# Kernel tuning notes

Measured on AMD Instinct MI355X. Metric: run time of the kernel, lower is better.

Reference implementation:

```python
import jax, jax.numpy as jnp
import numpy as np
import math

EMBED = 1024
HEADS = 16
HEAD_DIM = EMBED // HEADS
B, Hh, Ww = 256, 10, 10
MAX_POS = 100


def setup_inputs() -> dict:
    key = jax.random.key(0)
    ks = jax.random.split(key, 10)
    s = 1.0 / math.sqrt(EMBED)
    return {
        "x": jax.random.normal(ks[0], (B, EMBED, Hh, Ww), dtype=jnp.float32),
        "Wq": jax.random.uniform(ks[1], (EMBED, EMBED), jnp.float32, -s, s),
        "bq": jax.random.uniform(ks[2], (EMBED,), jnp.float32, -s, s),
        "Wk": jax.random.uniform(ks[3], (EMBED, EMBED), jnp.float32, -s, s),
        "bk": jax.random.uniform(ks[4], (EMBED,), jnp.float32, -s, s),
        "Wv": jax.random.uniform(ks[5], (EMBED, EMBED), jnp.float32, -s, s),
        "bv": jax.random.uniform(ks[6], (EMBED,), jnp.float32, -s, s),
        "Wo": jax.random.uniform(ks[7], (EMBED, EMBED), jnp.float32, -s, s),
        "bo": jax.random.uniform(ks[8], (EMBED,), jnp.float32, -s, s),
        "pos_encoding": jax.random.normal(ks[9], (MAX_POS, EMBED), dtype=jnp.float32),
    }


def reference(x, Wq, bq, Wk, bk, Wv, bv, Wo, bo, pos_encoding):
    # x: [B, E, H, W]
    b, e, h, w = x.shape
    s = h * w  # seq_len
    scale = math.sqrt(HEAD_DIM)
    x_flat = x.reshape(b, e, s).transpose(0, 2, 1)  # [B, S, E]
    x_flat = x_flat + pos_encoding[:s][None]  # broadcast over batch
    q = x_flat @ Wq + bq
    k = x_flat @ Wk + bk
    v = x_flat @ Wv + bv
    # [B, H, S, D]
    q = q.reshape(b, s, HEADS, HEAD_DIM).transpose(0, 2, 1, 3)
    k = k.reshape(b, s, HEADS, HEAD_DIM).transpose(0, 2, 1, 3)
    v = v.reshape(b, s, HEADS, HEAD_DIM).transpose(0, 2, 1, 3)
    scores = jnp.einsum('bhqd,bhkd->bhqk', q, k) / scale
    attn = jax.nn.softmax(scores, axis=-1)  # dropout = identity (eval)
    attended = jnp.einsum('bhqk,bhkd->bhqd', attn, v)
    attended = attended.transpose(0, 2, 1, 3).reshape(b, s, e)
    out = attended @ Wo + bo
    out = out.transpose(0, 2, 1).reshape(b, e, h, w)
    return out, attn
```

## Files before the change

### kernel.cpp

```cpp
#include <hip/hip_runtime.h>

typedef unsigned short u16;
typedef __attribute__((ext_vector_type(8))) short short8;
typedef __attribute__((ext_vector_type(4))) float f32x4;

#define BATCH 256
#define S_LEN 100
#define EMB   1024
#define NHEAD 16
#define HDIM  64

__device__ __forceinline__ float b2f(u16 h) {
  union { unsigned u; float f; } v; v.u = ((unsigned)h) << 16; return v.f;
}
__device__ __forceinline__ u16 f2bf(float f) {
  union { float f; unsigned u; } v; v.f = f;
  unsigned r = v.u + 0x7fffu + ((v.u >> 16) & 1u);
  return (u16)(r >> 16);
}

__device__ __forceinline__ void gld_lds16(const u16* g, u16* l) {
  __builtin_amdgcn_global_load_lds((const __attribute__((address_space(1))) void*)g,
                                   (__attribute__((address_space(3))) void*)l,
                                   16, 0, 0);
}

#define MFMA16(a, b, c) __builtin_amdgcn_mfma_f32_16x16x32_bf16(a, b, c, 0, 0, 0)

__global__ __launch_bounds__(256) void w_xpose(
    const float* __restrict__ Wq, const float* __restrict__ Wk,
    const float* __restrict__ Wv, const float* __restrict__ Wo,
    u16* __restrict__ WtQ, u16* __restrict__ WtK,
    u16* __restrict__ WtV, u16* __restrict__ WtO)
{
  __shared__ u16 tile[64 * 73];
  int z = blockIdx.z;
  const float* W = (z == 0) ? Wq : (z == 1) ? Wk : (z == 2) ? Wv : Wo;
  u16* Wt        = (z == 0) ? WtQ : (z == 1) ? WtK : (z == 2) ? WtV : WtO;
  int k0 = blockIdx.x * 64, n0 = blockIdx.y * 64;
  for (int idx = threadIdx.x; idx < 4096; idx += 256) {
    int r = idx >> 6, c = idx & 63;
    tile[r * 73 + c] = f2bf(W[(size_t)(k0 + r) * EMB + n0 + c]);
  }
  __syncthreads();
  for (int idx = threadIdx.x; idx < 4096; idx += 256) {
    int c = idx >> 6, r = idx & 63;
    Wt[(size_t)(n0 + c) * EMB + k0 + r] = tile[r * 73 + c];
  }
}

__global__ __launch_bounds__(256) void xpose_pos(
    const float* __restrict__ x, const float* __restrict__ pos, u16* __restrict__ xT)
{
  __shared__ float tile[64 * 105];
  int e0 = blockIdx.x * 64;
  int b  = blockIdx.y;
  const float* xb = x + (size_t)b * EMB * S_LEN;
  for (int idx = threadIdx.x; idx < 6400; idx += 256) {
    int i = idx / 100, s = idx - i * 100;
    tile[i * 105 + s] = xb[(size_t)(e0 + i) * S_LEN + s];
  }
  __syncthreads();
  for (int idx = threadIdx.x; idx < 6400; idx += 256) {
    int s = idx >> 6, i = idx & 63;
    float v = tile[i * 105 + s] + pos[(size_t)s * EMB + e0 + i];
    xT[(size_t)b * (S_LEN * EMB) + (size_t)s * EMB + e0 + i] = f2bf(v);
  }
}

__global__ __launch_bounds__(256) void out_xpose(
    const u16* __restrict__ tmp, float* __restrict__ out)
{
  __shared__ u16 tile[100 * 73];
  int e0 = blockIdx.x * 64;
  int b  = blockIdx.y;
  for (int idx = threadIdx.x; idx < 6400; idx += 256) {
    int s = idx >> 6, i = idx & 63;
    tile[s * 73 + i] = tmp[(size_t)b * (S_LEN * EMB) + (size_t)s * EMB + e0 + i];
  }
  __syncthreads();
  for (int idx = threadIdx.x; idx < 6400; idx += 256) {
    int i = idx / 100, s = idx - i * 100;
    out[((size_t)b * EMB + e0 + i) * S_LEN + s] = b2f(tile[s * 73 + i]);
  }
}

__global__ __launch_bounds__(512) void gemm256(
    const u16* __restrict__ A,
    const u16* __restrict__ Bt0, const u16* __restrict__ Bt1, const u16* __restrict__ Bt2,
    const float* __restrict__ bias0, const float* __restrict__ bias1, const float* __restrict__ bias2,
    u16* __restrict__ C0, u16* __restrict__ C1, u16* __restrict__ C2)
{
  __shared__ u16 lds[5 * 16384];

  const int z = blockIdx.z;
  const u16* Bt     = (z == 0) ? Bt0 : (z == 1) ? Bt1 : Bt2;
  const float* bias = (z == 0) ? bias0 : (z == 1) ? bias1 : bias2;
  u16* C            = (z == 0) ? C0 : (z == 1) ? C1 : C2;

  const int tid  = threadIdx.x;
  const int wave = tid >> 6, lane = tid & 63;
  const int quad = lane >> 4, l16 = lane & 15;
  const int m0 = blockIdx.x * 256, n0 = blockIdx.y * 256;
  const int WM = (wave >> 2) * 128, WN = (wave & 3) * 64;

  const int rq64 = tid >> 3;
  const int jg   = ((tid & 7) ^ (rq64 & 7)) << 3;

  const int swz = l16 & 7;
  const int cA  = (quad ^ swz) << 3;
  const int cB  = ((quad + 4) ^ swz) << 3;
  const int wmh = WM >> 7;
  const int wnh = WN >> 7;
  const int bRow = (WN & 127) + l16;

#define STAGE_SLOT(s, ri) { \
    const size_t kof = (size_t)((s) >> 1) * 64 + jg; \
    const int hof = 128 * ((s) & 1); \
    u16* dst = lds + (size_t)(ri) * 16384 + tid * 8; \
    gld_lds16(A  + (size_t)(m0 + hof + rq64)      * EMB + kof, dst); \
    gld_lds16(A  + (size_t)(m0 + hof + 64 + rq64) * EMB + kof, dst + 4096); \
    gld_lds16(Bt + (size_t)(n0 + hof + rq64)      * EMB + kof, dst + 8192); \
    gld_lds16(Bt + (size_t)(n0 + hof + 64 + rq64) * EMB + kof, dst + 12288); \
  }

  f32x4 acc[8][4] = {};

  STAGE_SLOT(0, 0); STAGE_SLOT(1, 1); STAGE_SLOT(2, 2);
  STAGE_SLOT(3, 3); STAGE_SLOT(4, 4);

  int ri0 = 0, ri1 = 1;
#pragma unroll 1
  for (int t = 0; t < 16; ++t) {
    if (t == 0) {
      asm volatile("s_waitcnt vmcnt(12)" ::: "memory");
    } else if (t == 15) {
      asm volatile("s_waitcnt vmcnt(0)" ::: "memory");
    } else {
      asm volatile("s_waitcnt vmcnt(4)" ::: "memory");
    }
    __builtin_amdgcn_s_barrier();

    if (t >= 1) {
      int s1 = 2 * t + 3;
      if (s1 <= 31) { int ia = ri1 + 2; if (ia >= 5) ia -= 5; STAGE_SLOT(s1, ia); }
      int s2 = 2 * t + 4;
      if (s2 <= 31) { int ib = ri1 + 3; if (ib >= 5) ib -= 5; STAGE_SLOT(s2, ib); }
    }

    const u16* sA = lds + (size_t)(wmh ? ri1 : ri0) * 16384;
    const u16* sB = lds + (size_t)(wnh ? ri1 : ri0) * 16384 + 8192;
    const u16* a0 = sA + l16 * 64 + cA;
    const u16* a1 = sA + l16 * 64 + cB;
    const u16* b0 = sB + bRow * 64 + cA;
    const u16* b1 = sB + bRow * 64 + cB;

    short8 bF[2][4];
#pragma unroll
    for (int ni = 0; ni < 4; ++ni) {
      bF[0][ni] = *(const short8*)(b0 + ni * 1024);
      bF[1][ni] = *(const short8*)(b1 + ni * 1024);
    }
    __builtin_amdgcn_s_setprio(1);
#pragma unroll
    for (int p = 0; p < 4; ++p) {
      short8 aF[2][2];
      aF[0][0] = *(const short8*)(a0 + (2 * p) * 1024);
      aF[0][1] = *(const short8*)(a1 + (2 * p) * 1024);
      aF[1][0] = *(const short8*)(a0 + (2 * p + 1) * 1024);
      aF[1][1] = *(const short8*)(a1 + (2 * p + 1) * 1024);
#pragma unroll
      for (int kh = 0; kh < 2; ++kh) {
#pragma unroll
        for (int ni = 0; ni < 4; ++ni) {
          acc[2 * p][ni]     = MFMA16(aF[0][kh], bF[kh][ni], acc[2 * p][ni]);
          acc[2 * p + 1][ni] = MFMA16(aF[1][kh], bF[kh][ni], acc[2 * p + 1][ni]);
        }
      }
    }
    __builtin_amdgcn_s_setprio(0);

    ri0 += 2; if (ri0 >= 5) ri0 -= 5;
    ri1 += 2; if (ri1 >= 5) ri1 -= 5;
  }

#pragma unroll
  for (int ni = 0; ni < 4; ++ni) {
    int col = n0 + WN + ni * 16 + l16;
    float bv = bias[col];
#pragma unroll
    for (int mi = 0; mi < 8; ++mi) {
#pragma unroll
      for (int r = 0; r < 4; ++r) {
        int row = m0 + WM + mi * 16 + quad * 4 + r;
        C[(size_t)row * EMB + col] = f2bf(acc[mi][ni][r] + bv);
      }
    }
  }
#undef STAGE_SLOT
}

__global__ __launch_bounds__(256) void attn_kernel(
    const u16* __restrict__ Q, const u16* __restrict__ Kb, const u16* __restrict__ V,
    float* __restrict__ attn_out, u16* __restrict__ attended)
{
  __shared__ u16 sQK[112 * 64 * 2];
  __shared__ __align__(16) char smemB[100 * 105 * 4];
  __shared__ float sRed[256];

  u16* sQ   = sQK;
  u16* sK   = sQK + 112 * 64;
  u16* sP   = sQK;
  float* sS = (float*)smemB;
  u16* sVt  = (u16*)smemB;

  const int bh = blockIdx.x;
  const int b = bh >> 4, h = bh & 15;
  const int tid = threadIdx.x;
  const int wave = tid >> 6, lane = tid & 63;
  const int quad = lane >> 4, l16 = lane & 15;
  const size_t qbase = (size_t)b * S_LEN * EMB + h * HDIM;

  uint4 vr0, vr1, vr2, vr3 = make_uint4(0, 0, 0, 0);
  {
    int c0 = tid, c1 = tid + 256, c2 = tid + 512;
    vr0 = *(const uint4*)(V + qbase + (size_t)(c0 >> 3) * EMB + ((c0 & 7) << 3));
    vr1 = *(const uint4*)(V + qbase + (size_t)(c1 >> 3) * EMB + ((c1 & 7) << 3));
    vr2 = *(const uint4*)(V + qbase + (size_t)(c2 >> 3) * EMB + ((c2 & 7) << 3));
    if (tid < 32) {
      int c3 = tid + 768;
      vr3 = *(const uint4*)(V + qbase + (size_t)(c3 >> 3) * EMB + ((c3 & 7) << 3));
    }
  }

  for (int c = tid; c < 896; c += 256) {
    int s = c >> 3, j = c & 7;
    int jg = (j ^ (s & 7)) << 3;
    uint4 qv = make_uint4(0, 0, 0, 0), kv = make_uint4(0, 0, 0, 0);
    if (s < S_LEN) {
      qv = *(const uint4*)(Q  + qbase + (size_t)s * EMB + jg);
      kv = *(const uint4*)(Kb + qbase + (size_t)s * EMB + jg);
    }
    *(uint4*)(sQ + c * 8) = qv;
    *(uint4*)(sK + c * 8) = kv;
  }
  __syncthreads();

  for (int t = wave; t < 49; t += 4) {
    int mi = t / 7, ni = t - mi * 7;
    f32x4 acc = {0.f, 0.f, 0.f, 0.f};
#pragma unroll
    for (int kk = 0; kk < 64; kk += 32) {
      int rq = mi * 16 + l16, rk = ni * 16 + l16;
      int cix = (kk >> 3) + quad;
      short8 a  = *(const short8*)(sQ + rq * 64 + ((cix ^ (rq & 7)) << 3));
      short8 bb = *(const short8*)(sK + rk * 64 + ((cix ^ (rk & 7)) << 3));
      acc = __builtin_amdgcn_mfma_f32_16x16x32_bf16(a, bb, acc, 0, 0, 0);
    }
    int col = ni * 16 + l16;
#pragma unroll
    for (int r = 0; r < 4; ++r) {
      int row = mi * 16 + quad * 4 + r;
      if (row < S_LEN && col < S_LEN) sS[row * 105 + col] = acc[r] * 0.125f;
    }
  }
  __syncthreads();

  for (int i = tid; i < 192; i += 256)
    *(uint4*)(sP + (100 + (i >> 4)) * 128 + ((i & 15) << 3)) = make_uint4(0, 0, 0, 0);

  if (tid < 200) {
    int row = tid >> 1, half = tid & 1;
    float* Srow = sS + row * 105;
    int c0 = half * 50, c1 = c0 + 50;
    float m0 = -1e30f, m1 = -1e30f;
    for (int c = c0; c < c1; c += 2) {
      m0 = fmaxf(m0, Srow[c]);
      m1 = fmaxf(m1, Srow[c + 1]);
    }
    sRed[tid] = fmaxf(m0, m1);
  }
  __syncthreads();
  if (tid < 200) {
    int row = tid >> 1, half = tid & 1;
    float* Srow = sS + row * 105;
    float mxv = fmaxf(sRed[row * 2], sRed[row * 2 + 1]);
    int c0 = half * 50, c1 = c0 + 50;
    float s0 = 0.f, s1 = 0.f;
    for (int c = c0; c < c1; c += 2) {
      float e0 = __expf(Srow[c] - mxv);
      float e1 = __expf(Srow[c + 1] - mxv);
      Srow[c] = e0; Srow[c + 1] = e1;
      s0 += e0; s1 += e1;
    }
    sRed[tid] = s0 + s1;
  }
  __syncthreads();
  if (tid < 200) {
    int row = tid >> 1, half = tid & 1;
    float* Srow = sS + row * 105;
    u16* Prow = sP + row * 128;
    int rs = row & 7;
    float inv = 1.f / (sRed[row * 2] + sRed[row * 2 + 1]);
    int c0 = half * 50, c1 = c0 + 50;
    for (int c = c0; c < c1; ++c) {
      float p = Srow[c] * inv;
      Srow[c] = p;
      Prow[(((c >> 3) ^ rs) << 3) + (c & 7)] = f2bf(p);
    }
    if (half == 1) {
      for (int c = S_LEN; c < 128; ++c)
        Prow[(((c >> 3) ^ rs) << 3) + (c & 7)] = 0;
    }
  }
  __syncthreads();

  {
    float* ao = attn_out + (size_t)bh * (S_LEN * S_LEN);
    for (int i = tid; i < S_LEN * S_LEN; i += 256) {
      int r = i / 100, c = i - r * 100;
      ao[i] = sS[r * 105 + c];
    }
  }
  __syncthreads();

  for (int i = tid; i < 1024; i += 256)
    *(uint4*)(sVt + i * 8) = make_uint4(0, 0, 0, 0);
  __syncthreads();
  {
    const u16* p0 = (const u16*)&vr0;
    const u16* p1 = (const u16*)&vr1;
    const u16* p2 = (const u16*)&vr2;
    const u16* p3 = (const u16*)&vr3;
    int c0 = tid, c1 = tid + 256, c2 = tid + 512, c3 = tid + 768;
#pragma unroll
    for (int j = 0; j < 8; ++j) {
      int s, d;
      s = c0 >> 3; d = ((c0 & 7) << 3) + j;
      sVt[d * 128 + (((s >> 3) ^ (d & 7)) << 3) + (s & 7)] = p0[j];
      s = c1 >> 3; d = ((c1 & 7) << 3) + j;
      sVt[d * 128 + (((s >> 3) ^ (d & 7)) << 3) + (s & 7)] = p1[j];
      s = c2 >> 3; d = ((c2 & 7) << 3) + j;
      sVt[d * 128 + (((s >> 3) ^ (d & 7)) << 3) + (s & 7)] = p2[j];
      if (tid < 32) {
        s = c3 >> 3; d = ((c3 & 7) << 3) + j;
        sVt[d * 128 + (((s >> 3) ^ (d & 7)) << 3) + (s & 7)] = p3[j];
      }
    }
  }
  __syncthreads();

  for (int t = wave; t < 28; t += 4) {
    int mi = t >> 2, ni = t & 3;
    f32x4 acc = {0.f, 0.f, 0.f, 0.f};
#pragma unroll
    for (int kk = 0; kk < 128; kk += 32) {
      int rp = mi * 16 + l16, rv = ni * 16 + l16;
      int cix = (kk >> 3) + quad;
      short8 a  = *(const short8*)(sP  + rp * 128 + ((cix ^ (rp & 7)) << 3));
      short8 bb = *(const short8*)(sVt + rv * 128 + ((cix ^ (rv & 7)) << 3));
      acc = __builtin_amdgcn_mfma_f32_16x16x32_bf16(a, bb, acc, 0, 0, 0);
    }
    int col = ni * 16 + l16;
#pragma unroll
    for (int r = 0; r < 4; ++r) {
      int row = mi * 16 + quad * 4 + r;
      if (row < S_LEN)
        attended[((size_t)b * S_LEN + row) * EMB + h * HDIM + col] = f2bf(acc[r]);
    }
  }
}

extern "C" void kernel_launch(void* const* d_in, const int* in_sizes, int n_in,
                              void* d_out, int out_size, void* d_ws, size_t ws_size,
                              hipStream_t stream) {
  const float* x   = (const float*)d_in[0];
  const float* Wq  = (const float*)d_in[1];
  const float* bq  = (const float*)d_in[2];
  const float* Wk  = (const float*)d_in[3];
  const float* bk  = (const float*)d_in[4];
  const float* Wv  = (const float*)d_in[5];
  const float* bv  = (const float*)d_in[6];
  const float* Wo  = (const float*)d_in[7];
  const float* bo  = (const float*)d_in[8];
  const float* pos = (const float*)d_in[9];

  float* out  = (float*)d_out;
  float* attn = out + (size_t)BATCH * EMB * S_LEN;

  const size_t MTOT = (size_t)BATCH * S_LEN;
  u16* ws   = (u16*)d_ws;
  u16* xT   = ws;
  u16* Qb   = ws + MTOT * EMB;
  u16* Kbuf = ws + 2 * MTOT * EMB;
  u16* Vb   = ws + 3 * MTOT * EMB;
  u16* WtQ  = ws + 4 * MTOT * EMB;
  u16* WtK  = WtQ + (size_t)EMB * EMB;
  u16* WtV  = WtK + (size_t)EMB * EMB;
  u16* WtO  = WtV + (size_t)EMB * EMB;
  u16* attended = xT;
  u16* tmp      = Qb;

  w_xpose<<<dim3(16, 16, 4), 256, 0, stream>>>(Wq, Wk, Wv, Wo, WtQ, WtK, WtV, WtO);
  xpose_pos<<<dim3(16, BATCH), 256, 0, stream>>>(x, pos, xT);
  gemm256<<<dim3(100, 4, 3), 512, 0, stream>>>(xT, WtQ, WtK, WtV, bq, bk, bv,
                                               Qb, Kbuf, Vb);
  attn_kernel<<<dim3(BATCH * NHEAD), 256, 0, stream>>>(Qb, Kbuf, Vb, attn, attended);
  gemm256<<<dim3(100, 4, 1), 512, 0, stream>>>(attended, WtO, WtO, WtO, bo, bo, bo,
                                               tmp, tmp, tmp);
  out_xpose<<<dim3(16, BATCH), 256, 0, stream>>>(tmp, out);
}
```

Before: 771.0 us.

## Restructure GEMM k-loop into barrier-synchronized phases with interleaved prefetch

Splits each k-iteration of the QKV GEMM into four phases. Each phase loads A fragments, optionally issues the next stage's global-to-LDS loads, then hits a block barrier and an lgkmcnt wait before its MFMA burst, ping-ponging the waves. The prologue now preloads three slots instead of five, and the vmcnt wait plus barrier move to the end of the last phase. The goal is to spread global load issue across the MFMA work and keep waves in lockstep so memory and math overlap. The cost is more barriers per iteration, which may stall waves, and a more fragile waitcnt accounting.

```diff
diff --git a/kernel.cpp b/kernel.cpp
--- a/kernel.cpp
+++ b/kernel.cpp
@@ -91,7 +91,7 @@
     const float* __restrict__ bias0, const float* __restrict__ bias1, const float* __restrict__ bias2,
     u16* __restrict__ C0, u16* __restrict__ C1, u16* __restrict__ C2)
 {
-  __shared__ u16 lds[5 * 16384];
+  __shared__ u16 ring[5][16384];
 
   const int z = blockIdx.z;
   const u16* Bt     = (z == 0) ? Bt0 : (z == 1) ? Bt1 : Bt2;
@@ -111,45 +111,54 @@
   const int cA  = (quad ^ swz) << 3;
   const int cB  = ((quad + 4) ^ swz) << 3;
   const int wmh = WM >> 7;
-  const int wnh = WN >> 7;
+  const int wnh = (wave & 3) >> 1;
   const int bRow = (WN & 127) + l16;
 
 #define STAGE_SLOT(s, ri) { \
     const size_t kof = (size_t)((s) >> 1) * 64 + jg; \
     const int hof = 128 * ((s) & 1); \
-    u16* dst = lds + (size_t)(ri) * 16384 + tid * 8; \
+    u16* dst = &ring[ri][tid * 8]; \
     gld_lds16(A  + (size_t)(m0 + hof + rq64)      * EMB + kof, dst); \
     gld_lds16(A  + (size_t)(m0 + hof + 64 + rq64) * EMB + kof, dst + 4096); \
     gld_lds16(Bt + (size_t)(n0 + hof + rq64)      * EMB + kof, dst + 8192); \
     gld_lds16(Bt + (size_t)(n0 + hof + 64 + rq64) * EMB + kof, dst + 12288); \
   }
 
+#define PHASE(j, PRE, GATE_, TAIL) { \
+    short8 aF[2][2]; \
+    aF[0][0] = *(const short8*)(a0 + (j) * 2048); \
+    aF[0][1] = *(const short8*)(a1 + (j) * 2048); \
+    aF[1][0] = *(const short8*)(a0 + (j) * 2048 + 1024); \
+    aF[1][1] = *(const short8*)(a1 + (j) * 2048 + 1024); \
+    PRE; \
+    GATE_; \
+    __builtin_amdgcn_s_barrier(); \
+    asm volatile("s_waitcnt lgkmcnt(0)" ::: "memory"); \
+    __builtin_amdgcn_sched_barrier(0); \
+    __builtin_amdgcn_s_setprio(1); \
+    _Pragma("unroll") \
+    for (int kh = 0; kh < 2; ++kh) { \
+      _Pragma("unroll") \
+      for (int ni = 0; ni < 4; ++ni) { \
+        acc[2 * (j)][ni]     = MFMA16(aF[0][kh], bF[kh][ni], acc[2 * (j)][ni]); \
+        acc[2 * (j) + 1][ni] = MFMA16(aF[1][kh], bF[kh][ni], acc[2 * (j) + 1][ni]); \
+      } \
+    } \
+    __builtin_amdgcn_s_setprio(0); \
+    TAIL; \
+  }
+
   f32x4 acc[8][4] = {};
 
   STAGE_SLOT(0, 0); STAGE_SLOT(1, 1); STAGE_SLOT(2, 2);
-  STAGE_SLOT(3, 3); STAGE_SLOT(4, 4);
-
-  int ri0 = 0, ri1 = 1;
+  asm volatile("s_waitcnt vmcnt(4)" ::: "memory");
+  __builtin_amdgcn_s_barrier();
+
+  int r0 = 0, r1 = 1;
 #pragma unroll 1
   for (int t = 0; t < 16; ++t) {
-    if (t == 0) {
-      asm volatile("s_waitcnt vmcnt(12)" ::: "memory");
-    } else if (t == 15) {
-      asm volatile("s_waitcnt vmcnt(0)" ::: "memory");
-    } else {
-      asm volatile("s_waitcnt vmcnt(4)" ::: "memory");
-    }
-    __builtin_amdgcn_s_barrier();
-
-    if (t >= 1) {
-      int s1 = 2 * t + 3;
-      if (s1 <= 31) { int ia = ri1 + 2; if (ia >= 5) ia -= 5; STAGE_SLOT(s1, ia); }
-      int s2 = 2 * t + 4;
-      if (s2 <= 31) { int ib = ri1 + 3; if (ib >= 5) ib -= 5; STAGE_SLOT(s2, ib); }
-    }
-
-    const u16* sA = lds + (size_t)(wmh ? ri1 : ri0) * 16384;
-    const u16* sB = lds + (size_t)(wnh ? ri1 : ri0) * 16384 + 8192;
+    const u16* sA = ring[wmh ? r1 : r0];
+    const u16* sB = ring[wnh ? r1 : r0] + 8192;
     const u16* a0 = sA + l16 * 64 + cA;
     const u16* a1 = sA + l16 * 64 + cB;
     const u16* b0 = sB + bRow * 64 + cA;
@@ -161,27 +170,26 @@
       bF[0][ni] = *(const short8*)(b0 + ni * 1024);
       bF[1][ni] = *(const short8*)(b1 + ni * 1024);
     }
-    __builtin_amdgcn_s_setprio(1);
-#pragma unroll
-    for (int p = 0; p < 4; ++p) {
-      short8 aF[2][2];
-      aF[0][0] = *(const short8*)(a0 + (2 * p) * 1024);
-      aF[0][1] = *(const short8*)(a1 + (2 * p) * 1024);
-      aF[1][0] = *(const short8*)(a0 + (2 * p + 1) * 1024);
-      aF[1][1] = *(const short8*)(a1 + (2 * p + 1) * 1024);
-#pragma unroll
-      for (int kh = 0; kh < 2; ++kh) {
-#pragma unroll
-        for (int ni = 0; ni < 4; ++ni) {
-          acc[2 * p][ni]     = MFMA16(aF[0][kh], bF[kh][ni], acc[2 * p][ni]);
-          acc[2 * p + 1][ni] = MFMA16(aF[1][kh], bF[kh][ni], acc[2 * p + 1][ni]);
-        }
-      }
-    }
-    __builtin_amdgcn_s_setprio(0);
-
-    ri0 += 2; if (ri0 >= 5) ri0 -= 5;
-    ri1 += 2; if (ri1 >= 5) ri1 -= 5;
+
+    int s3 = r1 + 2; if (s3 >= 5) s3 -= 5;
+    int s4 = r1 + 3; if (s4 >= 5) s4 -= 5;
+    const int k3 = 2 * t + 3, k4 = 2 * t + 4;
+
+    PHASE(0, { if (k3 <= 31) STAGE_SLOT(k3, s3); }, { (void)0; }, { (void)0; });
+    PHASE(1, { if (k4 <= 31) STAGE_SLOT(k4, s4); }, { (void)0; }, { (void)0; });
+    PHASE(2, { (void)0; }, { (void)0; }, { (void)0; });
+    if (t <= 13) {
+      PHASE(3, { (void)0; }, { asm volatile("s_waitcnt vmcnt(4)" ::: "memory"); },
+            { __builtin_amdgcn_s_barrier(); });
+    } else if (t == 14) {
+      PHASE(3, { (void)0; }, { asm volatile("s_waitcnt vmcnt(0)" ::: "memory"); },
+            { __builtin_amdgcn_s_barrier(); });
+    } else {
+      PHASE(3, { (void)0; }, { (void)0; }, { (void)0; });
+    }
+
+    r0 += 2; if (r0 >= 5) r0 -= 5;
+    r1 += 2; if (r1 >= 5) r1 -= 5;
   }
 
 #pragma unroll
@@ -197,6 +205,7 @@
       }
     }
   }
+#undef PHASE
 #undef STAGE_SLOT
 }
 
```

Measured after the change: 780.7 us. No clear change (+1.2%).
